# Optimization experiments

Hardware: AMD Instinct MI355X
Metric: run time of the kernel (lower is better)

The kernel has to match this reference:

```python
import jax, jax.numpy as jnp
import numpy as np

N = 100000
E = 3200000
NFEAT = 256
NHID = 128
NCLASS = 64


def setup_inputs() -> dict:
    key = jax.random.key(0)
    ks = jax.random.split(key, 10)
    x = jax.random.normal(ks[0], (N, NFEAT), dtype=jnp.float32)
    src = jax.random.randint(ks[1], (E,), 0, N, dtype=jnp.int32).astype(jnp.int64)
    dst = jax.random.randint(ks[2], (E,), 0, N, dtype=jnp.int32).astype(jnp.int64)
    # Glorot-ish init for GraphConv weights
    def w(k, i, o):
        return jax.random.normal(k, (i, o), dtype=jnp.float32) * (1.0 / np.sqrt(i))
    W0 = w(ks[3], NFEAT, NHID)
    b0 = jnp.zeros((NHID,), dtype=jnp.float32)
    W1 = w(ks[4], NHID, NHID)
    b1 = jnp.zeros((NHID,), dtype=jnp.float32)
    W2 = w(ks[5], NHID, NCLASS)
    b2 = jnp.zeros((NCLASS,), dtype=jnp.float32)
    return {"x": x, "src": src, "dst": dst,
            "W0": W0, "b0": b0, "W1": W1, "b1": b1, "W2": W2, "b2": b2}


def _degree_norms(src, dst, dtype):
    ones = jnp.ones(src.shape, dtype)
    deg_out = jax.ops.segment_sum(ones, src, num_segments=N)
    deg_in = jax.ops.segment_sum(ones, dst, num_segments=N)
    # clamp zero degrees to avoid inf (DGL clamps to 1)
    n_src = jnp.where(deg_out > 0, deg_out, 1.0) ** -0.5
    n_dst = jnp.where(deg_in > 0, deg_in, 1.0) ** -0.5
    return n_src, n_dst


def _graph_conv(h, src, dst, n_src, n_dst, W, b):
    # weight first (math-equivalent to DGL ordering), then normalized SpMM
    h = h @ W                              # [N, out]
    msg = h[src] * n_src[src][:, None]     # [E, out] gather + src norm
    agg = jax.ops.segment_sum(msg, dst, num_segments=N)  # [N, out]
    return agg * n_dst[:, None] + b


def reference(x, src, dst, W0, b0, W1, b1, W2, b2):
    n_src, n_dst = _degree_norms(src, dst, x.dtype)
    h = _graph_conv(x, src, dst, n_src, n_dst, W0, b0)
    # dropout is identity in eval mode
    h = _graph_conv(h, src, dst, n_src, n_dst, W1, b1)
    h = _graph_conv(h, src, dst, n_src, n_dst, W2, b2)
    return jax.nn.softmax(h, axis=1)
```

## Files before the change

### kernel.cpp

```cpp
#include <hip/hip_runtime.h>
#include <hip/hip_bf16.h>

#define N_NODES 100000
#define N_EDGES 3200000
#define NFEAT 256
#define NHID 128
#define NCLASS 64
#define SCAN_B 1024
#define NB_SCAN ((N_NODES + SCAN_B - 1) / SCAN_B)
#define NVEC4 (N_EDGES / 4)
#define RANGE (N_NODES / 8)
#define NSL 64

typedef unsigned int uint32;
typedef unsigned short ushort16;

static __device__ __forceinline__ float b2f(ushort16 u) {
    union { float f; uint32 i; } c; c.i = ((uint32)u) << 16; return c.f;
}
static __device__ __forceinline__ ushort16 f2b(float f) {
    union { float f; uint32 i; } c; c.f = f;
    uint32 r = (c.i + 0x7FFFu + ((c.i >> 16) & 1u)) >> 16;
    return (ushort16)r;
}
static __device__ __forceinline__ float blo(uint32 u) {
    union { float f; uint32 i; } c; c.i = u << 16; return c.f;
}
static __device__ __forceinline__ float bhi(uint32 u) {
    union { float f; uint32 i; } c; c.i = u & 0xFFFF0000u; return c.f;
}

__global__ __launch_bounds__(256) void k_hist(const int4* __restrict__ src4,
                                              const int4* __restrict__ dst4,
                                              uint32* __restrict__ scratch) {
    __shared__ uint32 h[RANGE];
    int g = blockIdx.x & 7, sl = blockIdx.x >> 3;
    int lo = g * RANGE, hi = lo + RANGE;
    for (int i = threadIdx.x; i < RANGE; i += 256) h[i] = 0u;
    __syncthreads();
    for (int t = sl * 256 + threadIdx.x; t < NVEC4; t += NSL * 256) {
        int4 s = src4[t], d = dst4[t];
        if (s.x >= lo && s.x < hi) atomicAdd(&h[s.x - lo], 1u);
        if (s.y >= lo && s.y < hi) atomicAdd(&h[s.y - lo], 1u);
        if (s.z >= lo && s.z < hi) atomicAdd(&h[s.z - lo], 1u);
        if (s.w >= lo && s.w < hi) atomicAdd(&h[s.w - lo], 1u);
        if (d.x >= lo && d.x < hi) atomicAdd(&h[d.x - lo], 65536u);
        if (d.y >= lo && d.y < hi) atomicAdd(&h[d.y - lo], 65536u);
        if (d.z >= lo && d.z < hi) atomicAdd(&h[d.z - lo], 65536u);
        if (d.w >= lo && d.w < hi) atomicAdd(&h[d.w - lo], 65536u);
    }
    __syncthreads();
    uint32* dstp = scratch + ((size_t)(g * NSL + sl)) * RANGE;
    for (int i = threadIdx.x; i < RANGE; i += 256) dstp[i] = h[i];
}

__global__ void k_sumdeg(const uint32* __restrict__ scratch, int* __restrict__ deg_in,
                         float* __restrict__ n_src, float* __restrict__ n_dst) {
    int i = blockIdx.x * blockDim.x + threadIdx.x;
    if (i >= N_NODES) return;
    int g = i / RANGE, r = i - g * RANGE;
    const uint32* base = scratch + (size_t)g * NSL * RANGE + r;
    uint32 so = 0, di = 0;
    for (int s = 0; s < NSL; s++) {
        uint32 v = base[(size_t)s * RANGE];
        so += v & 0xFFFFu;
        di += v >> 16;
    }
    deg_in[i] = (int)di;
    uint32 so1 = so < 1u ? 1u : so;
    uint32 di1 = di < 1u ? 1u : di;
    n_src[i] = rsqrtf((float)so1);
    n_dst[i] = rsqrtf((float)di1);
}

__global__ void k_scan1(const int* __restrict__ deg_in, int* __restrict__ row_ptr,
                        int* __restrict__ blk_sums) {
    __shared__ int sh[SCAN_B];
    int i = blockIdx.x * SCAN_B + threadIdx.x;
    int v = (i < N_NODES) ? deg_in[i] : 0;
    sh[threadIdx.x] = v;
    __syncthreads();
    for (int o = 1; o < SCAN_B; o <<= 1) {
        int t = 0;
        if ((int)threadIdx.x >= o) t = sh[threadIdx.x - o];
        __syncthreads();
        sh[threadIdx.x] += t;
        __syncthreads();
    }
    if (i < N_NODES) row_ptr[i] = sh[threadIdx.x] - v;
    if (threadIdx.x == SCAN_B - 1) blk_sums[blockIdx.x] = sh[SCAN_B - 1];
}

__global__ void k_scan2(int* __restrict__ blk_sums) {
    if (threadIdx.x == 0 && blockIdx.x == 0) {
        int acc = 0;
        for (int b = 0; b < NB_SCAN; b++) { int v = blk_sums[b]; blk_sums[b] = acc; acc += v; }
        blk_sums[NB_SCAN] = acc;
    }
}

__global__ void k_scan3(const int* __restrict__ blk_sums, int* __restrict__ row_ptr) {
    int i = blockIdx.x * SCAN_B + threadIdx.x;
    if (i < N_NODES) row_ptr[i] += blk_sums[blockIdx.x];
    if (i == 0) row_ptr[N_NODES] = blk_sums[NB_SCAN];
}

__global__ void k_offsets(uint32* __restrict__ scratch, const int* __restrict__ row_ptr) {
    int i = blockIdx.x * blockDim.x + threadIdx.x;
    if (i >= N_NODES) return;
    int g = i / RANGE, r = i - g * RANGE;
    uint32* base = scratch + (size_t)g * NSL * RANGE + r;
    uint32 run = (uint32)row_ptr[i];
    for (int s = 0; s < NSL; s++) {
        uint32 v = base[(size_t)s * RANGE];
        base[(size_t)s * RANGE] = run;
        run += v >> 16;
    }
}

__global__ __launch_bounds__(256) void k_fill2(const int4* __restrict__ src4,
                                               const int4* __restrict__ dst4,
                                               const uint32* __restrict__ scratch,
                                               int* __restrict__ col) {
    __shared__ uint32 cur[RANGE];
    int g = blockIdx.x & 7, sl = blockIdx.x >> 3;
    int lo = g * RANGE, hi = lo + RANGE;
    const uint32* base = scratch + ((size_t)(g * NSL + sl)) * RANGE;
    for (int i = threadIdx.x; i < RANGE; i += 256) cur[i] = base[i];
    __syncthreads();
    for (int t = sl * 256 + threadIdx.x; t < NVEC4; t += NSL * 256) {
        int4 s = src4[t], d = dst4[t];
        if (d.x >= lo && d.x < hi) { uint32 p = atomicAdd(&cur[d.x - lo], 1u); col[p] = s.x; }
        if (d.y >= lo && d.y < hi) { uint32 p = atomicAdd(&cur[d.y - lo], 1u); col[p] = s.y; }
        if (d.z >= lo && d.z < hi) { uint32 p = atomicAdd(&cur[d.z - lo], 1u); col[p] = s.z; }
        if (d.w >= lo && d.w < hi) { uint32 p = atomicAdd(&cur[d.w - lo], 1u); col[p] = s.w; }
    }
}

__global__ void k_w01(const float* __restrict__ W0, const float* __restrict__ W1,
                      float* __restrict__ W01) {
    __shared__ float row[NHID];
    int r = blockIdx.x, c = threadIdx.x;
    row[c] = W0[r * NHID + c];
    __syncthreads();
    float acc = 0.f;
    for (int k = 0; k < NHID; k++) acc += row[k] * W1[k * NHID + c];
    W01[r * NHID + c] = acc;
}

__global__ void k_wc(const float* __restrict__ W01, const float* __restrict__ W2,
                     float* __restrict__ Wc) {
    __shared__ float row[NHID];
    int r = blockIdx.x, c = threadIdx.x;
    row[c] = W01[r * NHID + c];
    row[c + 64] = W01[r * NHID + c + 64];
    __syncthreads();
    float acc = 0.f;
    for (int k = 0; k < NHID; k++) acc += row[k] * W2[k * NCLASS + c];
    Wc[r * NCLASS + c] = acc;
}

__global__ void k_bv(const float* __restrict__ b0, const float* __restrict__ W1,
                     const float* __restrict__ b1, const float* __restrict__ W2,
                     float* __restrict__ bv) {
    __shared__ float tmp[NHID];
    int c = threadIdx.x;
    for (int cc = c; cc < NHID; cc += 64) {
        float a = 0.f;
        for (int k = 0; k < NHID; k++) a += b0[k] * W1[k * NHID + cc];
        tmp[cc] = a;
    }
    __syncthreads();
    float a1 = 0.f, a2 = 0.f;
    for (int k = 0; k < NHID; k++) {
        float wv = W2[k * NCLASS + c];
        a1 += tmp[k] * wv;
        a2 += b1[k] * wv;
    }
    bv[c] = a1;
    bv[64 + c] = a2;
}

static __device__ __forceinline__ void fma4(float4& a, float xs, const float4& wv) {
    a.x += xs * wv.x; a.y += xs * wv.y; a.z += xs * wv.z; a.w += xs * wv.w;
}
__global__ __launch_bounds__(256) void k_gemm_y(const float* __restrict__ x,
                                                const float* __restrict__ Wc,
                                                ushort16* __restrict__ y) {
    __shared__ float w_sh[128][NCLASS];
    int tid = threadIdx.x;
    int tx = tid & 15, ty = tid >> 4;
    int row0 = blockIdx.x * 64 + ty * 4;
    int c0 = tx * 4;
    int r0 = min(row0 + 0, N_NODES - 1);
    int r1 = min(row0 + 1, N_NODES - 1);
    int r2 = min(row0 + 2, N_NODES - 1);
    int r3 = min(row0 + 3, N_NODES - 1);
    const float* xp0 = x + (size_t)r0 * NFEAT;
    const float* xp1 = x + (size_t)r1 * NFEAT;
    const float* xp2 = x + (size_t)r2 * NFEAT;
    const float* xp3 = x + (size_t)r3 * NFEAT;
    const float4* wsrc = (const float4*)Wc;
    float4* wdst = (float4*)&w_sh[0][0];
    float4 acc0 = {0, 0, 0, 0}, acc1 = {0, 0, 0, 0}, acc2 = {0, 0, 0, 0}, acc3 = {0, 0, 0, 0};
    float4 xa = *(const float4*)(xp0);
    float4 xb = *(const float4*)(xp1);
    float4 xc = *(const float4*)(xp2);
    float4 xd = *(const float4*)(xp3);
#pragma unroll
    for (int half = 0; half < 2; half++) {
        const int kb = half * 128;
        if (half) __syncthreads();
        for (int i = tid; i < 128 * NCLASS / 4; i += 256)
            wdst[i] = wsrc[kb * (NCLASS / 4) + i];
        __syncthreads();
#pragma unroll 4
        for (int k = kb; k < kb + 128; k += 4) {
            float4 ca = xa, cb = xb, cc = xc, cd = xd;
            if (k + 4 < NFEAT) {
                xa = *(const float4*)(xp0 + k + 4);
                xb = *(const float4*)(xp1 + k + 4);
                xc = *(const float4*)(xp2 + k + 4);
                xd = *(const float4*)(xp3 + k + 4);
            }
            int kl = k - kb;
            float4 w0 = *(const float4*)&w_sh[kl + 0][c0];
            float4 w1 = *(const float4*)&w_sh[kl + 1][c0];
            float4 w2 = *(const float4*)&w_sh[kl + 2][c0];
            float4 w3 = *(const float4*)&w_sh[kl + 3][c0];
            fma4(acc0, ca.x, w0); fma4(acc0, ca.y, w1); fma4(acc0, ca.z, w2); fma4(acc0, ca.w, w3);
            fma4(acc1, cb.x, w0); fma4(acc1, cb.y, w1); fma4(acc1, cb.z, w2); fma4(acc1, cb.w, w3);
            fma4(acc2, cc.x, w0); fma4(acc2, cc.y, w1); fma4(acc2, cc.z, w2); fma4(acc2, cc.w, w3);
            fma4(acc3, cd.x, w0); fma4(acc3, cd.y, w1); fma4(acc3, cd.z, w2); fma4(acc3, cd.w, w3);
        }
    }
    ushort4 o0 = {f2b(acc0.x), f2b(acc0.y), f2b(acc0.z), f2b(acc0.w)};
    ushort4 o1 = {f2b(acc1.x), f2b(acc1.y), f2b(acc1.z), f2b(acc1.w)};
    ushort4 o2 = {f2b(acc2.x), f2b(acc2.y), f2b(acc2.z), f2b(acc2.w)};
    ushort4 o3 = {f2b(acc3.x), f2b(acc3.y), f2b(acc3.z), f2b(acc3.w)};
    if (row0 + 0 < N_NODES) *(ushort4*)(y + (size_t)(row0 + 0) * NCLASS + c0) = o0;
    if (row0 + 1 < N_NODES) *(ushort4*)(y + (size_t)(row0 + 1) * NCLASS + c0) = o1;
    if (row0 + 2 < N_NODES) *(ushort4*)(y + (size_t)(row0 + 2) * NCLASS + c0) = o2;
    if (row0 + 3 < N_NODES) *(ushort4*)(y + (size_t)(row0 + 3) * NCLASS + c0) = o3;
}

template <int PASS>
__global__ __launch_bounds__(256) void k_agg(
        const int* __restrict__ row_ptr, const int* __restrict__ col,
        const float* __restrict__ n_src, const float* __restrict__ n_dst,
        const ushort16* __restrict__ in, ushort16* __restrict__ out,
        float* __restrict__ outf,
        const float* __restrict__ tin, float* __restrict__ tout,
        const float* __restrict__ t1, const float* __restrict__ t2,
        const float* __restrict__ bv, const float* __restrict__ b2) {
    int wid = threadIdx.x >> 6, lane = threadIdx.x & 63;
    int node = blockIdx.x * 4 + wid;
    if (node >= N_NODES) return;
    int g = lane >> 3, sub = lane & 7;
    int s = row_ptr[node], e = row_ptr[node + 1];
    const uint4* inr = (const uint4*)in;

    float acc0 = 0.f, acc1 = 0.f, acc2 = 0.f, acc3 = 0.f;
    float acc4 = 0.f, acc5 = 0.f, acc6 = 0.f, acc7 = 0.f;
    float accs = 0.f;

#define CH(P)                                                                  \
    {                                                                          \
        int p_ = (P);                                                          \
        bool v_ = p_ < e;                                                      \
        int j_ = v_ ? col[p_] : 0;                                             \
        float ns_ = n_src[j_];                                                 \
        if (!v_) ns_ = 0.f;                                                    \
        uint4 u_ = inr[(size_t)j_ * 8 + sub];                                  \
        acc0 += ns_ * blo(u_.x); acc1 += ns_ * bhi(u_.x);                      \
        acc2 += ns_ * blo(u_.y); acc3 += ns_ * bhi(u_.y);                      \
        acc4 += ns_ * blo(u_.z); acc5 += ns_ * bhi(u_.z);                      \
        acc6 += ns_ * blo(u_.w); acc7 += ns_ * bhi(u_.w);                      \
        if (PASS == 1) accs += ns_;                                            \
        if (PASS == 2) accs += ns_ * tin[j_];                                  \
    }

    for (int base = s; base < e; base += 32) {
        CH(base + g)
        CH(base + 8 + g)
        CH(base + 16 + g)
        CH(base + 24 + g)
    }
#undef CH

#pragma unroll
    for (int off = 8; off <= 32; off <<= 1) {
        acc0 += __shfl_xor(acc0, off, 64);
        acc1 += __shfl_xor(acc1, off, 64);
        acc2 += __shfl_xor(acc2, off, 64);
        acc3 += __shfl_xor(acc3, off, 64);
        acc4 += __shfl_xor(acc4, off, 64);
        acc5 += __shfl_xor(acc5, off, 64);
        acc6 += __shfl_xor(acc6, off, 64);
        acc7 += __shfl_xor(acc7, off, 64);
        if (PASS != 3) accs += __shfl_xor(accs, off, 64);
    }

    float nd = n_dst[node];
    if (PASS == 3) {
        float t2n = t2[node], t1n = t1[node];
        const float* bvA = bv + sub * 8;
        const float* bvB = bv + 64 + sub * 8;
        const float* b2p = b2 + sub * 8;
        float v0 = acc0 * nd + t2n * bvA[0] + t1n * bvB[0] + b2p[0];
        float v1 = acc1 * nd + t2n * bvA[1] + t1n * bvB[1] + b2p[1];
        float v2 = acc2 * nd + t2n * bvA[2] + t1n * bvB[2] + b2p[2];
        float v3 = acc3 * nd + t2n * bvA[3] + t1n * bvB[3] + b2p[3];
        float v4 = acc4 * nd + t2n * bvA[4] + t1n * bvB[4] + b2p[4];
        float v5 = acc5 * nd + t2n * bvA[5] + t1n * bvB[5] + b2p[5];
        float v6 = acc6 * nd + t2n * bvA[6] + t1n * bvB[6] + b2p[6];
        float v7 = acc7 * nd + t2n * bvA[7] + t1n * bvB[7] + b2p[7];
        float m = fmaxf(fmaxf(fmaxf(v0, v1), fmaxf(v2, v3)),
                        fmaxf(fmaxf(v4, v5), fmaxf(v6, v7)));
#pragma unroll
        for (int off = 1; off <= 4; off <<= 1) m = fmaxf(m, __shfl_xor(m, off, 64));
        float e0 = __expf(v0 - m), e1 = __expf(v1 - m), e2 = __expf(v2 - m), e3 = __expf(v3 - m);
        float e4 = __expf(v4 - m), e5 = __expf(v5 - m), e6 = __expf(v6 - m), e7 = __expf(v7 - m);
        float sum = ((e0 + e1) + (e2 + e3)) + ((e4 + e5) + (e6 + e7));
#pragma unroll
        for (int off = 1; off <= 4; off <<= 1) sum += __shfl_xor(sum, off, 64);
        float r = 1.0f / sum;
        if (g == 0) {
            float4 o0 = {e0 * r, e1 * r, e2 * r, e3 * r};
            float4 o1 = {e4 * r, e5 * r, e6 * r, e7 * r};
            float4* op = (float4*)(outf + (size_t)node * NCLASS + sub * 8);
            op[0] = o0;
            op[1] = o1;
        }
    } else {
        if (g == 0) {
            uint32 w0 = (uint32)f2b(acc0 * nd) | ((uint32)f2b(acc1 * nd) << 16);
            uint32 w1 = (uint32)f2b(acc2 * nd) | ((uint32)f2b(acc3 * nd) << 16);
            uint32 w2 = (uint32)f2b(acc4 * nd) | ((uint32)f2b(acc5 * nd) << 16);
            uint32 w3 = (uint32)f2b(acc6 * nd) | ((uint32)f2b(acc7 * nd) << 16);
            uint4 w = {w0, w1, w2, w3};
            *((uint4*)(out + (size_t)node * NCLASS) + sub) = w;
        }
        if (lane == 0) tout[node] = accs * nd;
    }
}

extern "C" void kernel_launch(void* const* d_in, const int* in_sizes, int n_in,
                              void* d_out, int out_size, void* d_ws, size_t ws_size,
                              hipStream_t stream) {
    const float* x   = (const float*)d_in[0];
    const int*   src = (const int*)d_in[1];
    const int*   dst = (const int*)d_in[2];
    const float* W0  = (const float*)d_in[3];
    const float* b0  = (const float*)d_in[4];
    const float* W1  = (const float*)d_in[5];
    const float* b1  = (const float*)d_in[6];
    const float* W2  = (const float*)d_in[7];
    const float* b2  = (const float*)d_in[8];
    float* out = (float*)d_out;

    size_t off = 0;
    auto alloc = [&](size_t bytes) {
        void* p = (char*)d_ws + off;
        off = (off + bytes + 255) & ~(size_t)255;
        return p;
    };
    int*      deg_in   = (int*)alloc(N_NODES * 4);
    float*    n_src    = (float*)alloc(N_NODES * 4);
    float*    n_dst    = (float*)alloc(N_NODES * 4);
    int*      row_ptr  = (int*)alloc((N_NODES + 1) * 4);
    int*      blk_sums = (int*)alloc((NB_SCAN + 1) * 4);
    int*      col      = (int*)alloc((size_t)N_EDGES * 4);
    uint32*   scratch  = (uint32*)alloc((size_t)8 * NSL * RANGE * 4);
    float*    W01      = (float*)alloc(NFEAT * NHID * 4);
    float*    Wc       = (float*)alloc(NFEAT * NCLASS * 4);
    float*    bv       = (float*)alloc(128 * 4);
    float*    t1       = (float*)alloc(N_NODES * 4);
    float*    t2       = (float*)alloc(N_NODES * 4);
    ushort16* bufB1    = (ushort16*)alloc((size_t)N_NODES * NCLASS * 2);
    ushort16* bufB2    = (ushort16*)alloc((size_t)N_NODES * NCLASS * 2);
    (void)ws_size; (void)in_sizes; (void)n_in; (void)out_size;

    const int TB = 256;
    const int NBn = (N_NODES + TB - 1) / TB;
    const int NW = (N_NODES + 3) / 4;
    const int GP = 8 * NSL;

    k_hist<<<GP, TB, 0, stream>>>((const int4*)src, (const int4*)dst, scratch);
    k_sumdeg<<<NBn, TB, 0, stream>>>(scratch, deg_in, n_src, n_dst);
    k_scan1<<<NB_SCAN, SCAN_B, 0, stream>>>(deg_in, row_ptr, blk_sums);
    k_scan2<<<1, 64, 0, stream>>>(blk_sums);
    k_scan3<<<NB_SCAN, SCAN_B, 0, stream>>>(blk_sums, row_ptr);
    k_offsets<<<NBn, TB, 0, stream>>>(scratch, row_ptr);
    k_fill2<<<GP, TB, 0, stream>>>((const int4*)src, (const int4*)dst, scratch, col);

    k_w01<<<NFEAT, NHID, 0, stream>>>(W0, W1, W01);
    k_wc<<<NFEAT, NCLASS, 0, stream>>>(W01, W2, Wc);
    k_bv<<<1, NCLASS, 0, stream>>>(b0, W1, b1, W2, bv);

    k_gemm_y<<<(N_NODES + 63) / 64, 256, 0, stream>>>(x, Wc, bufB1);

    k_agg<1><<<NW, 256, 0, stream>>>(row_ptr, col, n_src, n_dst, bufB1, bufB2, nullptr,
                                     nullptr, t1, nullptr, nullptr, nullptr, nullptr);
    k_agg<2><<<NW, 256, 0, stream>>>(row_ptr, col, n_src, n_dst, bufB2, bufB1, nullptr,
                                     t1, t2, nullptr, nullptr, nullptr, nullptr);
    k_agg<3><<<NW, 256, 0, stream>>>(row_ptr, col, n_src, n_dst, bufB1, nullptr, out,
                                     nullptr, nullptr, t1, t2, bv, b2);
}
```

Baseline: 577.8 us.

## Use bf16 MFMA for the input projection GEMM with transposed bf16 weights

Replaces the FP32 shared-memory FMA GEMM (x @ Wc) with a per-wavefront 16x16x32 bf16 MFMA kernel. x is converted to bf16 in registers and the combined weight is stored transposed in bf16 so each lane can load B fragments directly from global memory. This cuts ALU cost in the projection, but the GEMM over 100k x 256 is mostly memory-bound on reading x. It also adds bf16 rounding of the inputs and uses scattered 2-byte output stores.

```diff
diff --git a/kernel.cpp b/kernel.cpp
--- a/kernel.cpp
+++ b/kernel.cpp
@@ -14,6 +14,8 @@
 
 typedef unsigned int uint32;
 typedef unsigned short ushort16;
+typedef __attribute__((ext_vector_type(8))) short bf16x8;
+typedef __attribute__((ext_vector_type(4))) float f32x4;
 
 static __device__ __forceinline__ float b2f(ushort16 u) {
     union { float f; uint32 i; } c; c.i = ((uint32)u) << 16; return c.f;
@@ -149,7 +151,7 @@
 }
 
 __global__ void k_wc(const float* __restrict__ W01, const float* __restrict__ W2,
-                     float* __restrict__ Wc) {
+                     float* __restrict__ Wc, ushort16* __restrict__ Wt) {
     __shared__ float row[NHID];
     int r = blockIdx.x, c = threadIdx.x;
     row[c] = W01[r * NHID + c];
@@ -158,6 +160,7 @@
     float acc = 0.f;
     for (int k = 0; k < NHID; k++) acc += row[k] * W2[k * NCLASS + c];
     Wc[r * NCLASS + c] = acc;
+    Wt[(size_t)c * NFEAT + r] = f2b(acc);
 }
 
 __global__ void k_bv(const float* __restrict__ b0, const float* __restrict__ W1,
@@ -181,67 +184,58 @@
     bv[64 + c] = a2;
 }
 
-static __device__ __forceinline__ void fma4(float4& a, float xs, const float4& wv) {
-    a.x += xs * wv.x; a.y += xs * wv.y; a.z += xs * wv.z; a.w += xs * wv.w;
-}
 __global__ __launch_bounds__(256) void k_gemm_y(const float* __restrict__ x,
-                                                const float* __restrict__ Wc,
+                                                const ushort16* __restrict__ Wt,
                                                 ushort16* __restrict__ y) {
-    __shared__ float w_sh[128][NCLASS];
     int tid = threadIdx.x;
-    int tx = tid & 15, ty = tid >> 4;
-    int row0 = blockIdx.x * 64 + ty * 4;
-    int c0 = tx * 4;
-    int r0 = min(row0 + 0, N_NODES - 1);
-    int r1 = min(row0 + 1, N_NODES - 1);
-    int r2 = min(row0 + 2, N_NODES - 1);
-    int r3 = min(row0 + 3, N_NODES - 1);
-    const float* xp0 = x + (size_t)r0 * NFEAT;
-    const float* xp1 = x + (size_t)r1 * NFEAT;
-    const float* xp2 = x + (size_t)r2 * NFEAT;
-    const float* xp3 = x + (size_t)r3 * NFEAT;
-    const float4* wsrc = (const float4*)Wc;
-    float4* wdst = (float4*)&w_sh[0][0];
-    float4 acc0 = {0, 0, 0, 0}, acc1 = {0, 0, 0, 0}, acc2 = {0, 0, 0, 0}, acc3 = {0, 0, 0, 0};
-    float4 xa = *(const float4*)(xp0);
-    float4 xb = *(const float4*)(xp1);
-    float4 xc = *(const float4*)(xp2);
-    float4 xd = *(const float4*)(xp3);
-#pragma unroll
-    for (int half = 0; half < 2; half++) {
-        const int kb = half * 128;
-        if (half) __syncthreads();
-        for (int i = tid; i < 128 * NCLASS / 4; i += 256)
-            wdst[i] = wsrc[kb * (NCLASS / 4) + i];
-        __syncthreads();
-#pragma unroll 4
-        for (int k = kb; k < kb + 128; k += 4) {
-            float4 ca = xa, cb = xb, cc = xc, cd = xd;
-            if (k + 4 < NFEAT) {
-                xa = *(const float4*)(xp0 + k + 4);
-                xb = *(const float4*)(xp1 + k + 4);
-                xc = *(const float4*)(xp2 + k + 4);
-                xd = *(const float4*)(xp3 + k + 4);
-            }
-            int kl = k - kb;
-            float4 w0 = *(const float4*)&w_sh[kl + 0][c0];
-            float4 w1 = *(const float4*)&w_sh[kl + 1][c0];
-            float4 w2 = *(const float4*)&w_sh[kl + 2][c0];
-            float4 w3 = *(const float4*)&w_sh[kl + 3][c0];
-            fma4(acc0, ca.x, w0); fma4(acc0, ca.y, w1); fma4(acc0, ca.z, w2); fma4(acc0, ca.w, w3);
-            fma4(acc1, cb.x, w0); fma4(acc1, cb.y, w1); fma4(acc1, cb.z, w2); fma4(acc1, cb.w, w3);
-            fma4(acc2, cc.x, w0); fma4(acc2, cc.y, w1); fma4(acc2, cc.z, w2); fma4(acc2, cc.w, w3);
-            fma4(acc3, cd.x, w0); fma4(acc3, cd.y, w1); fma4(acc3, cd.z, w2); fma4(acc3, cd.w, w3);
+    int wid = tid >> 6, lane = tid & 63;
+    int q = lane >> 4, r = lane & 15;
+    int rowbase = blockIdx.x * 64 + wid * 16;
+    int rowld = min(rowbase + r, N_NODES - 1);
+    const float* xp = x + (size_t)rowld * NFEAT + q * 8;
+
+    float4 alo[8], ahi[8];
+#pragma unroll
+    for (int kt = 0; kt < 8; kt++) {
+        alo[kt] = *(const float4*)(xp + kt * 32);
+        ahi[kt] = *(const float4*)(xp + kt * 32 + 4);
+    }
+
+    f32x4 acc0 = {0.f, 0.f, 0.f, 0.f};
+    f32x4 acc1 = {0.f, 0.f, 0.f, 0.f};
+    f32x4 acc2 = {0.f, 0.f, 0.f, 0.f};
+    f32x4 acc3 = {0.f, 0.f, 0.f, 0.f};
+
+#pragma unroll
+    for (int kt = 0; kt < 8; kt++) {
+        bf16x8 af;
+        af[0] = (short)f2b(alo[kt].x); af[1] = (short)f2b(alo[kt].y);
+        af[2] = (short)f2b(alo[kt].z); af[3] = (short)f2b(alo[kt].w);
+        af[4] = (short)f2b(ahi[kt].x); af[5] = (short)f2b(ahi[kt].y);
+        af[6] = (short)f2b(ahi[kt].z); af[7] = (short)f2b(ahi[kt].w);
+        const int ko = kt * 32 + q * 8;
+        bf16x8 b0 = *(const bf16x8*)(Wt + (size_t)(0 * 16 + r) * NFEAT + ko);
+        bf16x8 b1 = *(const bf16x8*)(Wt + (size_t)(1 * 16 + r) * NFEAT + ko);
+        bf16x8 b2 = *(const bf16x8*)(Wt + (size_t)(2 * 16 + r) * NFEAT + ko);
+        bf16x8 b3 = *(const bf16x8*)(Wt + (size_t)(3 * 16 + r) * NFEAT + ko);
+        acc0 = __builtin_amdgcn_mfma_f32_16x16x32_bf16(af, b0, acc0, 0, 0, 0);
+        acc1 = __builtin_amdgcn_mfma_f32_16x16x32_bf16(af, b1, acc1, 0, 0, 0);
+        acc2 = __builtin_amdgcn_mfma_f32_16x16x32_bf16(af, b2, acc2, 0, 0, 0);
+        acc3 = __builtin_amdgcn_mfma_f32_16x16x32_bf16(af, b3, acc3, 0, 0, 0);
+    }
+
+    int srow0 = rowbase + q * 4;
+#pragma unroll
+    for (int i = 0; i < 4; i++) {
+        int rr = srow0 + i;
+        if (rr < N_NODES) {
+            ushort16* yp = y + (size_t)rr * NCLASS + r;
+            yp[0]  = f2b(acc0[i]);
+            yp[16] = f2b(acc1[i]);
+            yp[32] = f2b(acc2[i]);
+            yp[48] = f2b(acc3[i]);
         }
     }
-    ushort4 o0 = {f2b(acc0.x), f2b(acc0.y), f2b(acc0.z), f2b(acc0.w)};
-    ushort4 o1 = {f2b(acc1.x), f2b(acc1.y), f2b(acc1.z), f2b(acc1.w)};
-    ushort4 o2 = {f2b(acc2.x), f2b(acc2.y), f2b(acc2.z), f2b(acc2.w)};
-    ushort4 o3 = {f2b(acc3.x), f2b(acc3.y), f2b(acc3.z), f2b(acc3.w)};
-    if (row0 + 0 < N_NODES) *(ushort4*)(y + (size_t)(row0 + 0) * NCLASS + c0) = o0;
-    if (row0 + 1 < N_NODES) *(ushort4*)(y + (size_t)(row0 + 1) * NCLASS + c0) = o1;
-    if (row0 + 2 < N_NODES) *(ushort4*)(y + (size_t)(row0 + 2) * NCLASS + c0) = o2;
-    if (row0 + 3 < N_NODES) *(ushort4*)(y + (size_t)(row0 + 3) * NCLASS + c0) = o3;
 }
 
 template <int PASS>
@@ -374,6 +368,7 @@
     uint32*   scratch  = (uint32*)alloc((size_t)8 * NSL * RANGE * 4);
     float*    W01      = (float*)alloc(NFEAT * NHID * 4);
     float*    Wc       = (float*)alloc(NFEAT * NCLASS * 4);
+    ushort16* Wt       = (ushort16*)alloc((size_t)NFEAT * NCLASS * 2);
     float*    bv       = (float*)alloc(128 * 4);
     float*    t1       = (float*)alloc(N_NODES * 4);
     float*    t2       = (float*)alloc(N_NODES * 4);
@@ -395,10 +390,10 @@
     k_fill2<<<GP, TB, 0, stream>>>((const int4*)src, (const int4*)dst, scratch, col);
 
     k_w01<<<NFEAT, NHID, 0, stream>>>(W0, W1, W01);
-    k_wc<<<NFEAT, NCLASS, 0, stream>>>(W01, W2, Wc);
+    k_wc<<<NFEAT, NCLASS, 0, stream>>>(W01, W2, Wc, Wt);
     k_bv<<<1, NCLASS, 0, stream>>>(b0, W1, b1, W2, bv);
 
-    k_gemm_y<<<(N_NODES + 63) / 64, 256, 0, stream>>>(x, Wc, bufB1);
+    k_gemm_y<<<(N_NODES + 63) / 64, 256, 0, stream>>>(x, Wt, bufB1);
 
     k_agg<1><<<NW, 256, 0, stream>>>(row_ptr, col, n_src, n_dst, bufB1, bufB2, nullptr,
                                      nullptr, t1, nullptr, nullptr, nullptr, nullptr);
```

Result: faster. 539.0 us (-6.7%).
